# Kernel tuning notes

Hardware: AMD Instinct MI355X
Metric: run time of the kernel (lower is better)

Reference implementation:

```python
import jax, jax.numpy as jnp
import numpy as np

WS = (2, 6, 12)            # window (z, h, w)
DIM = 192
HEADS = 6
Z_WINS = 8 // WS[0]        # 4
H_WINS = 96 // WS[1]       # 16
W_WINS = 180 // WS[2]      # 15
NUM_WINDOWS = Z_WINS * H_WINS  # 64 (bias-sharing groups)


def _position_index(ws):
    # Faithful numpy port of define_3d_earth_position_index (Pangu-Weather).
    z, h, w = ws
    czi = np.arange(z)
    czj = -np.arange(z) * z
    chi = np.arange(h)
    chj = -np.arange(h) * h
    cw = np.arange(w)
    c1 = np.stack(np.meshgrid(czi, chi, cw, indexing='ij')).reshape(3, -1)
    c2 = np.stack(np.meshgrid(czj, chj, cw, indexing='ij')).reshape(3, -1)
    coords = (c1[:, :, None] - c2[:, None, :]).transpose(1, 2, 0).astype(np.int64)
    coords[:, :, 2] += w - 1
    coords[:, :, 1] *= 2 * w - 1
    coords[:, :, 0] *= (2 * w - 1) * h * h
    return coords.sum(-1).astype(np.int32)  # (L, L)


def setup_inputs() -> dict:
    key = jax.random.key(0)
    ks = jax.random.split(key, 6)
    L = WS[0] * WS[1] * WS[2]                 # 144
    total = NUM_WINDOWS * W_WINS              # 960 windows (b=1)
    table_len = (2 * WS[2] - 1) * WS[1] ** 2 * WS[0] ** 2  # 3312
    x = jax.random.normal(ks[0], (total, L, DIM), jnp.float32)
    mask = jax.random.normal(ks[1], (total, L, L), jnp.float32)
    W1 = jax.random.normal(ks[2], (DIM, 3 * DIM), jnp.float32) * 0.02
    b1 = jnp.zeros((3 * DIM,), jnp.float32)
    W2 = jax.random.normal(ks[3], (DIM, DIM), jnp.float32) * 0.02
    b2 = jnp.zeros((DIM,), jnp.float32)
    bias_table = jax.random.normal(ks[4], (table_len, NUM_WINDOWS, HEADS), jnp.float32) * 0.02
    position_index = jnp.asarray(_position_index(WS))
    return {"x": x, "mask": mask, "W1": W1, "b1": b1, "W2": W2, "b2": b2,
            "bias_table": bias_table, "position_index": position_index,
            "b": 1, "z": Z_WINS, "h": H_WINS}


def reference(x, mask, W1, b1, W2, b2, bias_table, position_index, b, z, h):
    B_, L, C = x.shape                     # (b*nw*w_wins, 144, 192)
    hd = C // HEADS
    scale = hd ** -0.5
    nw = bias_table.shape[1]

    qkv = (x @ W1 + b1).reshape(B_, L, 3, HEADS, hd)
    qkv = qkv.transpose(2, 0, 3, 1, 4)      # (3, B_, H, L, hd)
    q, k, v = qkv[0] * scale, qkv[1], qkv[2]

    attn = jnp.einsum('bhld,bhmd->bhlm', q, k)  # (B_, H, L, L)

    # Earth-specific bias: gather then (nw, H, L, L)
    bias = bias_table[position_index]           # (L, L, nw, H)
    bias = bias.transpose(2, 3, 0, 1)           # (nw, H, L, L)

    # window ordering is (b, nw, w_wins); bias broadcasts over w_wins
    attn = attn.reshape(b, nw, -1, HEADS, L, L) + bias[None, :, None]
    attn = attn.reshape(b, -1, HEADS, L, L)
    attn = attn + mask[None, :, None]           # mask: (total, L, L)
    attn = attn.reshape(B_, HEADS, L, L)

    attn = jax.nn.softmax(attn, axis=-1)        # dropout p=0.0 -> identity

    out = jnp.einsum('bhlm,bhmd->bhld', attn, v)
    out = out.transpose(0, 2, 1, 3).reshape(B_, L, C)
    out = out @ W2 + b2
    return out
```

## Files before the change

kernel.cpp:

```cpp
#include <hip/hip_runtime.h>
#include <hip/hip_bf16.h>

typedef __bf16 bf16_t;
typedef __attribute__((ext_vector_type(8))) __bf16 bf16x8;
typedef __attribute__((ext_vector_type(4))) __bf16 bf16x4;
typedef __attribute__((ext_vector_type(4))) float f32x4;

#define LQ 144
#define CDIM 192
#define NHEADS 6
#define HD 32
#define NWIN 960
#define WWINS 15
#define MROWS 138240
#define SCALE_Q 0.17677669529663687f

#define OFF_QKV   0ull
#define OFF_ATTN  159252480ull
#define OFF_BIAS  212336640ull
#define OFF_W1T   244187136ull
#define OFF_W2T   244408320ull

__global__ void prep_w_kernel(const float* __restrict__ W1, const float* __restrict__ W2,
                              bf16_t* __restrict__ w1t, bf16_t* __restrict__ w2t) {
    int idx = blockIdx.x * 256 + threadIdx.x;
    if (idx < 576 * 192) {
        int n = idx / 192, k = idx % 192;
        w1t[idx] = (bf16_t)W1[k * 576 + n];
    }
    if (idx < 192 * 192) {
        int n = idx / 192, k = idx % 192;
        w2t[idx] = (bf16_t)W2[k * 192 + n];
    }
}

__global__ void bias_gather_kernel(const float* __restrict__ table, const int* __restrict__ pi,
                                   float* __restrict__ bias_full) {
    int idx = blockIdx.x * 256 + threadIdx.x;
    int m = idx % LQ;
    int t = idx / LQ;
    int q = t % LQ; t /= LQ;
    int hh = t % NHEADS;
    int nw = t / NHEADS;
    int p = pi[q * LQ + m];
    bias_full[idx] = table[(p * 64 + nw) * NHEADS + hh];
}

__global__ __launch_bounds__(256) void gemm1_kernel(
    const float* __restrict__ X, const bf16_t* __restrict__ W1t,
    const float* __restrict__ b1, bf16_t* __restrict__ qkv) {
    __shared__ bf16_t As[128 * 72];
    __shared__ bf16_t Bs[64 * 72];
    const int tid = threadIdx.x;
    const int row0 = blockIdx.x * 128;
    const int n0 = blockIdx.y * 64;
    const int lane = tid & 63, wid = tid >> 6;
    const int wr = wid >> 1, wc = wid & 1;
    const int l15 = lane & 15, g = lane >> 4;

    f32x4 acc[4][2];
#pragma unroll
    for (int a = 0; a < 4; ++a)
#pragma unroll
        for (int b = 0; b < 2; ++b) acc[a][b] = (f32x4){0.f, 0.f, 0.f, 0.f};

    for (int kk = 0; kk < 3; ++kk) {
        {
            int row = tid >> 1, half = tid & 1;
            const float* src = X + (size_t)(row0 + row) * 192 + kk * 64 + half * 32;
            bf16_t* dst = &As[row * 72 + half * 32];
#pragma unroll
            for (int j = 0; j < 4; ++j) {
                f32x4 v0 = ((const f32x4*)src)[2 * j];
                f32x4 v1 = ((const f32x4*)src)[2 * j + 1];
                bf16x8 w;
#pragma unroll
                for (int r = 0; r < 4; ++r) { w[r] = (bf16_t)v0[r]; w[4 + r] = (bf16_t)v1[r]; }
                *(bf16x8*)(dst + 8 * j) = w;
            }
        }
        {
            int n = tid >> 2, qtr = tid & 3;
            const bf16_t* src = W1t + (size_t)(n0 + n) * 192 + kk * 64 + qtr * 16;
            bf16x8 v0 = ((const bf16x8*)src)[0];
            bf16x8 v1 = ((const bf16x8*)src)[1];
            *(bf16x8*)&Bs[n * 72 + qtr * 16] = v0;
            *(bf16x8*)&Bs[n * 72 + qtr * 16 + 8] = v1;
        }
        __syncthreads();
#pragma unroll
        for (int ks = 0; ks < 2; ++ks) {
            bf16x8 af[4], bfr[2];
#pragma unroll
            for (int rt = 0; rt < 4; ++rt)
                af[rt] = *(const bf16x8*)&As[(wr * 64 + rt * 16 + l15) * 72 + ks * 32 + 8 * g];
#pragma unroll
            for (int ct = 0; ct < 2; ++ct)
                bfr[ct] = *(const bf16x8*)&Bs[(wc * 32 + ct * 16 + l15) * 72 + ks * 32 + 8 * g];
#pragma unroll
            for (int rt = 0; rt < 4; ++rt)
#pragma unroll
                for (int ct = 0; ct < 2; ++ct)
                    acc[rt][ct] = __builtin_amdgcn_mfma_f32_16x16x32_bf16(af[rt], bfr[ct], acc[rt][ct], 0, 0, 0);
        }
        __syncthreads();
    }
#pragma unroll
    for (int ct = 0; ct < 2; ++ct) {
        int n = n0 + wc * 32 + ct * 16 + l15;
        float bv = b1[n];
        float sc = (n < 192) ? SCALE_Q : 1.0f;
#pragma unroll
        for (int rt = 0; rt < 4; ++rt) {
#pragma unroll
            for (int r = 0; r < 4; ++r) {
                int m = row0 + wr * 64 + rt * 16 + 4 * g + r;
                qkv[(size_t)m * 576 + n] = (bf16_t)((acc[rt][ct][r] + bv) * sc);
            }
        }
    }
}

#define QKP 40
#define PP 168
__global__ __launch_bounds__(192) void attn_kernel(
    const bf16_t* __restrict__ qkv, const float* __restrict__ mask,
    const float* __restrict__ bias_full, bf16_t* __restrict__ attn_o) {
    __shared__ bf16_t Vt[32 * PP];
    __shared__ bf16_t Pb[144 * PP];
    bf16_t* Qs = Pb;
    bf16_t* Ks = Pb + 144 * QKP;

    const int tid = threadIdx.x;
    const int bid = blockIdx.x;
    const int wi = bid / NHEADS;
    const int h = bid % NHEADS;
    const int gb = (wi / WWINS) * NHEADS + h;

    const bf16_t* base = qkv + (size_t)wi * (LQ * 576);
#pragma unroll
    for (int it = 0; it < 3; ++it) {
        int idx = tid + it * 192;
        int l = idx >> 2, sg = (idx & 3) * 8;
        const bf16_t* p = base + l * 576 + h * 32 + sg;
        bf16x8 vq = *(const bf16x8*)(p);
        bf16x8 vk = *(const bf16x8*)(p + 192);
        bf16x8 vv = *(const bf16x8*)(p + 384);
        *(bf16x8*)&Qs[l * QKP + sg] = vq;
        *(bf16x8*)&Ks[l * QKP + sg] = vk;
#pragma unroll
        for (int j = 0; j < 8; ++j) Vt[(sg + j) * PP + l] = vv[j];
    }
    for (int idx = tid; idx < 512; idx += 192)
        Vt[(idx >> 4) * PP + 144 + (idx & 15)] = (bf16_t)0.f;
    __syncthreads();

    const int lane = tid & 63;
    const int wid = tid >> 6;
    const int l15 = lane & 15;
    const int g = lane >> 4;
    const int q0w = wid * 48;

    bf16x8 qf[3];
#pragma unroll
    for (int qt = 0; qt < 3; ++qt)
        qf[qt] = *(const bf16x8*)&Qs[(q0w + qt * 16 + l15) * QKP + 8 * g];

    f32x4 acc[3][9];
#pragma unroll
    for (int qt = 0; qt < 3; ++qt)
#pragma unroll
        for (int mt = 0; mt < 9; ++mt) acc[qt][mt] = (f32x4){0.f, 0.f, 0.f, 0.f};

#pragma unroll
    for (int mt = 0; mt < 9; ++mt) {
        bf16x8 kf = *(const bf16x8*)&Ks[(mt * 16 + l15) * QKP + 8 * g];
#pragma unroll
        for (int qt = 0; qt < 3; ++qt)
            acc[qt][mt] = __builtin_amdgcn_mfma_f32_16x16x32_bf16(kf, qf[qt], acc[qt][mt], 0, 0, 0);
    }
#pragma unroll
    for (int qt = 0; qt < 3; ++qt) {
        int q = q0w + qt * 16 + l15;
        const f32x4* brow = (const f32x4*)(bias_full + ((size_t)gb * LQ + q) * LQ);
        const f32x4* mrow = (const f32x4*)(mask + ((size_t)wi * LQ + q) * LQ);
#pragma unroll
        for (int mt = 0; mt < 9; ++mt) {
            f32x4 bv = brow[mt * 4 + g];
            f32x4 mv = mrow[mt * 4 + g];
            acc[qt][mt] += bv + mv;
        }
    }
    __syncthreads();

#pragma unroll
    for (int qt = 0; qt < 3; ++qt) {
        float mx = -3.0e38f;
#pragma unroll
        for (int mt = 0; mt < 9; ++mt)
#pragma unroll
            for (int r = 0; r < 4; ++r) mx = fmaxf(mx, acc[qt][mt][r]);
        mx = fmaxf(mx, __shfl_xor(mx, 16));
        mx = fmaxf(mx, __shfl_xor(mx, 32));
        float sum = 0.f;
#pragma unroll
        for (int mt = 0; mt < 9; ++mt)
#pragma unroll
            for (int r = 0; r < 4; ++r) {
                float e = __expf(acc[qt][mt][r] - mx);
                acc[qt][mt][r] = e;
                sum += e;
            }
        sum += __shfl_xor(sum, 16);
        sum += __shfl_xor(sum, 32);
        float inv = 1.f / sum;
        int q = q0w + qt * 16 + l15;
#pragma unroll
        for (int mt = 0; mt < 9; ++mt) {
            bf16x4 pk;
#pragma unroll
            for (int r = 0; r < 4; ++r) pk[r] = (bf16_t)(acc[qt][mt][r] * inv);
            *(bf16x4*)&Pb[q * PP + mt * 16 + 4 * g] = pk;
        }
    }
    {
        bf16x4 z; 
#pragma unroll
        for (int r = 0; r < 4; ++r) z[r] = (bf16_t)0.f;
#pragma unroll
        for (int u = 0; u < 3; ++u) {
            int uu = lane + u * 64;
            int row = q0w + (uu >> 2);
            *(bf16x4*)&Pb[row * PP + 144 + (uu & 3) * 4] = z;
        }
    }
    __syncthreads();

    f32x4 o[2][3];
#pragma unroll
    for (int dt = 0; dt < 2; ++dt)
#pragma unroll
        for (int qt = 0; qt < 3; ++qt) o[dt][qt] = (f32x4){0.f, 0.f, 0.f, 0.f};
#pragma unroll
    for (int mc = 0; mc < 5; ++mc) {
        bf16x8 av[2], bp[3];
#pragma unroll
        for (int dt = 0; dt < 2; ++dt)
            av[dt] = *(const bf16x8*)&Vt[(dt * 16 + l15) * PP + mc * 32 + 8 * g];
#pragma unroll
        for (int qt = 0; qt < 3; ++qt)
            bp[qt] = *(const bf16x8*)&Pb[(q0w + qt * 16 + l15) * PP + mc * 32 + 8 * g];
#pragma unroll
        for (int dt = 0; dt < 2; ++dt)
#pragma unroll
            for (int qt = 0; qt < 3; ++qt)
                o[dt][qt] = __builtin_amdgcn_mfma_f32_16x16x32_bf16(av[dt], bp[qt], o[dt][qt], 0, 0, 0);
    }
#pragma unroll
    for (int dt = 0; dt < 2; ++dt)
#pragma unroll
        for (int qt = 0; qt < 3; ++qt) {
            int q = q0w + qt * 16 + l15;
            int d0 = dt * 16 + 4 * g;
            bf16x4 pk;
#pragma unroll
            for (int r = 0; r < 4; ++r) pk[r] = (bf16_t)o[dt][qt][r];
            *(bf16x4*)(attn_o + ((size_t)wi * LQ + q) * CDIM + h * HD + d0) = pk;
        }
}

__global__ __launch_bounds__(256) void gemm2_kernel(
    const bf16_t* __restrict__ A, const bf16_t* __restrict__ W2t,
    const float* __restrict__ b2, float* __restrict__ out) {
    __shared__ bf16_t As[128 * 72];
    __shared__ bf16_t Bs[64 * 72];
    const int tid = threadIdx.x;
    const int row0 = blockIdx.x * 128;
    const int n0 = blockIdx.y * 64;
    const int lane = tid & 63, wid = tid >> 6;
    const int wr = wid >> 1, wc = wid & 1;
    const int l15 = lane & 15, g = lane >> 4;

    f32x4 acc[4][2];
#pragma unroll
    for (int a = 0; a < 4; ++a)
#pragma unroll
        for (int b = 0; b < 2; ++b) acc[a][b] = (f32x4){0.f, 0.f, 0.f, 0.f};

    for (int kk = 0; kk < 3; ++kk) {
        {
            int row = tid >> 1, half = tid & 1;
            const bf16_t* src = A + (size_t)(row0 + row) * 192 + kk * 64 + half * 32;
            bf16_t* dst = &As[row * 72 + half * 32];
            bf16x8 v0 = ((const bf16x8*)src)[0];
            bf16x8 v1 = ((const bf16x8*)src)[1];
            bf16x8 v2 = ((const bf16x8*)src)[2];
            bf16x8 v3 = ((const bf16x8*)src)[3];
            *(bf16x8*)(dst) = v0; *(bf16x8*)(dst + 8) = v1;
            *(bf16x8*)(dst + 16) = v2; *(bf16x8*)(dst + 24) = v3;
        }
        {
            int n = tid >> 2, qtr = tid & 3;
            const bf16_t* src = W2t + (size_t)(n0 + n) * 192 + kk * 64 + qtr * 16;
            bf16x8 v0 = ((const bf16x8*)src)[0];
            bf16x8 v1 = ((const bf16x8*)src)[1];
            *(bf16x8*)&Bs[n * 72 + qtr * 16] = v0;
            *(bf16x8*)&Bs[n * 72 + qtr * 16 + 8] = v1;
        }
        __syncthreads();
#pragma unroll
        for (int ks = 0; ks < 2; ++ks) {
            bf16x8 af[4], bfr[2];
#pragma unroll
            for (int rt = 0; rt < 4; ++rt)
                af[rt] = *(const bf16x8*)&As[(wr * 64 + rt * 16 + l15) * 72 + ks * 32 + 8 * g];
#pragma unroll
            for (int ct = 0; ct < 2; ++ct)
                bfr[ct] = *(const bf16x8*)&Bs[(wc * 32 + ct * 16 + l15) * 72 + ks * 32 + 8 * g];
#pragma unroll
            for (int rt = 0; rt < 4; ++rt)
#pragma unroll
                for (int ct = 0; ct < 2; ++ct)
                    acc[rt][ct] = __builtin_amdgcn_mfma_f32_16x16x32_bf16(af[rt], bfr[ct], acc[rt][ct], 0, 0, 0);
        }
        __syncthreads();
    }
#pragma unroll
    for (int ct = 0; ct < 2; ++ct) {
        int n = n0 + wc * 32 + ct * 16 + l15;
        float bv = b2[n];
#pragma unroll
        for (int rt = 0; rt < 4; ++rt) {
#pragma unroll
            for (int r = 0; r < 4; ++r) {
                int m = row0 + wr * 64 + rt * 16 + 4 * g + r;
                out[(size_t)m * 192 + n] = acc[rt][ct][r] + bv;
            }
        }
    }
}

extern "C" void kernel_launch(void* const* d_in, const int* in_sizes, int n_in,
                              void* d_out, int out_size, void* d_ws, size_t ws_size,
                              hipStream_t stream) {
    const float* x = (const float*)d_in[0];
    const float* mask = (const float*)d_in[1];
    const float* W1 = (const float*)d_in[2];
    const float* b1 = (const float*)d_in[3];
    const float* W2 = (const float*)d_in[4];
    const float* b2 = (const float*)d_in[5];
    const float* table = (const float*)d_in[6];
    const int* pi = (const int*)d_in[7];
    float* out = (float*)d_out;

    char* ws = (char*)d_ws;
    bf16_t* qkv = (bf16_t*)(ws + OFF_QKV);
    bf16_t* attn_o = (bf16_t*)(ws + OFF_ATTN);
    float* bias_full = (float*)(ws + OFF_BIAS);
    bf16_t* w1t = (bf16_t*)(ws + OFF_W1T);
    bf16_t* w2t = (bf16_t*)(ws + OFF_W2T);

    prep_w_kernel<<<dim3(432), dim3(256), 0, stream>>>(W1, W2, w1t, w2t);
    bias_gather_kernel<<<dim3(31104), dim3(256), 0, stream>>>(table, pi, bias_full);
    gemm1_kernel<<<dim3(1080, 9), dim3(256), 0, stream>>>(x, w1t, b1, qkv);
    attn_kernel<<<dim3(5760), dim3(192), 0, stream>>>(qkv, mask, bias_full, attn_o);
    gemm2_kernel<<<dim3(1080, 3), dim3(256), 0, stream>>>(attn_o, w2t, b2, out);
}
```

Baseline: 699.5 us.

## Split attention block into nine waves, one 16-row query tile each

The attention kernel now launches 576 threads (9 waves) per window-head, so each wave handles one 16-row query tile instead of three. Q fragments are loaded straight from global memory into registers rather than staged through shared memory, and K and V are loaded by all threads in a single pass. The aim is to raise the number of waves available to hide the latency of the bias and mask global loads and the softmax, and to lower per-thread register use. The cost is more barrier participants per block and fewer MFMAs per wave to amortize shared-memory fragment loads.

```diff
diff --git a/kernel.cpp b/kernel.cpp
--- a/kernel.cpp
+++ b/kernel.cpp
@@ -121,85 +121,66 @@
     }
 }
 
-#define QKP 40
+#define KP 40
 #define PP 168
-__global__ __launch_bounds__(192) void attn_kernel(
+__global__ __launch_bounds__(576) void attn_kernel(
     const bf16_t* __restrict__ qkv, const float* __restrict__ mask,
     const float* __restrict__ bias_full, bf16_t* __restrict__ attn_o) {
-    __shared__ bf16_t Vt[32 * PP];
-    __shared__ bf16_t Pb[144 * PP];
-    bf16_t* Qs = Pb;
-    bf16_t* Ks = Pb + 144 * QKP;
+    __shared__ bf16_t smem[176 * PP];
+    bf16_t* Pb = smem;
+    bf16_t* Vt = smem + 144 * PP;
+    bf16_t* Ks = smem;
 
     const int tid = threadIdx.x;
     const int bid = blockIdx.x;
     const int wi = bid / NHEADS;
     const int h = bid % NHEADS;
     const int gb = (wi / WWINS) * NHEADS + h;
-
     const bf16_t* base = qkv + (size_t)wi * (LQ * 576);
-#pragma unroll
-    for (int it = 0; it < 3; ++it) {
-        int idx = tid + it * 192;
-        int l = idx >> 2, sg = (idx & 3) * 8;
-        const bf16_t* p = base + l * 576 + h * 32 + sg;
-        bf16x8 vq = *(const bf16x8*)(p);
-        bf16x8 vk = *(const bf16x8*)(p + 192);
-        bf16x8 vv = *(const bf16x8*)(p + 384);
-        *(bf16x8*)&Qs[l * QKP + sg] = vq;
-        *(bf16x8*)&Ks[l * QKP + sg] = vk;
+
+    {
+        int l = tid >> 2, sg = (tid & 3) * 8;
+        const bf16_t* p = base + l * 576 + 192 + h * HD + sg;
+        bf16x8 vk = *(const bf16x8*)(p);
+        bf16x8 vv = *(const bf16x8*)(p + 192);
+        *(bf16x8*)&Ks[l * KP + sg] = vk;
 #pragma unroll
         for (int j = 0; j < 8; ++j) Vt[(sg + j) * PP + l] = vv[j];
     }
-    for (int idx = tid; idx < 512; idx += 192)
-        Vt[(idx >> 4) * PP + 144 + (idx & 15)] = (bf16_t)0.f;
-    __syncthreads();
+    if (tid < 512) Vt[(tid >> 4) * PP + 144 + (tid & 15)] = (bf16_t)0.f;
 
     const int lane = tid & 63;
     const int wid = tid >> 6;
     const int l15 = lane & 15;
     const int g = lane >> 4;
-    const int q0w = wid * 48;
-
-    bf16x8 qf[3];
-#pragma unroll
-    for (int qt = 0; qt < 3; ++qt)
-        qf[qt] = *(const bf16x8*)&Qs[(q0w + qt * 16 + l15) * QKP + 8 * g];
-
-    f32x4 acc[3][9];
-#pragma unroll
-    for (int qt = 0; qt < 3; ++qt)
-#pragma unroll
-        for (int mt = 0; mt < 9; ++mt) acc[qt][mt] = (f32x4){0.f, 0.f, 0.f, 0.f};
-
+    const int q = wid * 16 + l15;
+
+    bf16x8 qf = *(const bf16x8*)(base + q * 576 + h * HD + 8 * g);
+    __syncthreads();
+
+    f32x4 acc[9];
+#pragma unroll
+    for (int mt = 0; mt < 9; ++mt) acc[mt] = (f32x4){0.f, 0.f, 0.f, 0.f};
 #pragma unroll
     for (int mt = 0; mt < 9; ++mt) {
-        bf16x8 kf = *(const bf16x8*)&Ks[(mt * 16 + l15) * QKP + 8 * g];
-#pragma unroll
-        for (int qt = 0; qt < 3; ++qt)
-            acc[qt][mt] = __builtin_amdgcn_mfma_f32_16x16x32_bf16(kf, qf[qt], acc[qt][mt], 0, 0, 0);
-    }
-#pragma unroll
-    for (int qt = 0; qt < 3; ++qt) {
-        int q = q0w + qt * 16 + l15;
+        bf16x8 kf = *(const bf16x8*)&Ks[(mt * 16 + l15) * KP + 8 * g];
+        acc[mt] = __builtin_amdgcn_mfma_f32_16x16x32_bf16(kf, qf, acc[mt], 0, 0, 0);
+    }
+    {
         const f32x4* brow = (const f32x4*)(bias_full + ((size_t)gb * LQ + q) * LQ);
         const f32x4* mrow = (const f32x4*)(mask + ((size_t)wi * LQ + q) * LQ);
 #pragma unroll
-        for (int mt = 0; mt < 9; ++mt) {
-            f32x4 bv = brow[mt * 4 + g];
-            f32x4 mv = mrow[mt * 4 + g];
-            acc[qt][mt] += bv + mv;
-        }
+        for (int mt = 0; mt < 9; ++mt)
+            acc[mt] += brow[mt * 4 + g] + mrow[mt * 4 + g];
     }
     __syncthreads();
 
-#pragma unroll
-    for (int qt = 0; qt < 3; ++qt) {
+    {
         float mx = -3.0e38f;
 #pragma unroll
         for (int mt = 0; mt < 9; ++mt)
 #pragma unroll
-            for (int r = 0; r < 4; ++r) mx = fmaxf(mx, acc[qt][mt][r]);
+            for (int r = 0; r < 4; ++r) mx = fmaxf(mx, acc[mt][r]);
         mx = fmaxf(mx, __shfl_xor(mx, 16));
         mx = fmaxf(mx, __shfl_xor(mx, 32));
         float sum = 0.f;
@@ -207,66 +188,49 @@
         for (int mt = 0; mt < 9; ++mt)
 #pragma unroll
             for (int r = 0; r < 4; ++r) {
-                float e = __expf(acc[qt][mt][r] - mx);
-                acc[qt][mt][r] = e;
+                float e = __expf(acc[mt][r] - mx);
+                acc[mt][r] = e;
                 sum += e;
             }
         sum += __shfl_xor(sum, 16);
         sum += __shfl_xor(sum, 32);
         float inv = 1.f / sum;
-        int q = q0w + qt * 16 + l15;
 #pragma unroll
         for (int mt = 0; mt < 9; ++mt) {
             bf16x4 pk;
 #pragma unroll
-            for (int r = 0; r < 4; ++r) pk[r] = (bf16_t)(acc[qt][mt][r] * inv);
+            for (int r = 0; r < 4; ++r) pk[r] = (bf16_t)(acc[mt][r] * inv);
             *(bf16x4*)&Pb[q * PP + mt * 16 + 4 * g] = pk;
         }
     }
     {
-        bf16x4 z; 
+        bf16x4 z;
 #pragma unroll
         for (int r = 0; r < 4; ++r) z[r] = (bf16_t)0.f;
-#pragma unroll
-        for (int u = 0; u < 3; ++u) {
-            int uu = lane + u * 64;
-            int row = q0w + (uu >> 2);
-            *(bf16x4*)&Pb[row * PP + 144 + (uu & 3) * 4] = z;
-        }
+        int row = wid * 16 + (lane >> 2);
+        *(bf16x4*)&Pb[row * PP + 144 + (lane & 3) * 4] = z;
     }
     __syncthreads();
 
-    f32x4 o[2][3];
-#pragma unroll
-    for (int dt = 0; dt < 2; ++dt)
-#pragma unroll
-        for (int qt = 0; qt < 3; ++qt) o[dt][qt] = (f32x4){0.f, 0.f, 0.f, 0.f};
+    f32x4 o[2];
+#pragma unroll
+    for (int dt = 0; dt < 2; ++dt) o[dt] = (f32x4){0.f, 0.f, 0.f, 0.f};
 #pragma unroll
     for (int mc = 0; mc < 5; ++mc) {
-        bf16x8 av[2], bp[3];
-#pragma unroll
-        for (int dt = 0; dt < 2; ++dt)
-            av[dt] = *(const bf16x8*)&Vt[(dt * 16 + l15) * PP + mc * 32 + 8 * g];
-#pragma unroll
-        for (int qt = 0; qt < 3; ++qt)
-            bp[qt] = *(const bf16x8*)&Pb[(q0w + qt * 16 + l15) * PP + mc * 32 + 8 * g];
-#pragma unroll
-        for (int dt = 0; dt < 2; ++dt)
-#pragma unroll
-            for (int qt = 0; qt < 3; ++qt)
-                o[dt][qt] = __builtin_amdgcn_mfma_f32_16x16x32_bf16(av[dt], bp[qt], o[dt][qt], 0, 0, 0);
-    }
-#pragma unroll
-    for (int dt = 0; dt < 2; ++dt)
-#pragma unroll
-        for (int qt = 0; qt < 3; ++qt) {
-            int q = q0w + qt * 16 + l15;
-            int d0 = dt * 16 + 4 * g;
-            bf16x4 pk;
-#pragma unroll
-            for (int r = 0; r < 4; ++r) pk[r] = (bf16_t)o[dt][qt][r];
-            *(bf16x4*)(attn_o + ((size_t)wi * LQ + q) * CDIM + h * HD + d0) = pk;
-        }
+        bf16x8 bp = *(const bf16x8*)&Pb[q * PP + mc * 32 + 8 * g];
+#pragma unroll
+        for (int dt = 0; dt < 2; ++dt) {
+            bf16x8 av = *(const bf16x8*)&Vt[(dt * 16 + l15) * PP + mc * 32 + 8 * g];
+            o[dt] = __builtin_amdgcn_mfma_f32_16x16x32_bf16(av, bp, o[dt], 0, 0, 0);
+        }
+    }
+#pragma unroll
+    for (int dt = 0; dt < 2; ++dt) {
+        bf16x4 pk;
+#pragma unroll
+        for (int r = 0; r < 4; ++r) pk[r] = (bf16_t)o[dt][r];
+        *(bf16x4*)(attn_o + ((size_t)wi * LQ + q) * CDIM + h * HD + dt * 16 + 4 * g) = pk;
+    }
 }
 
 __global__ __launch_bounds__(256) void gemm2_kernel(
@@ -363,6 +327,6 @@
     prep_w_kernel<<<dim3(432), dim3(256), 0, stream>>>(W1, W2, w1t, w2t);
     bias_gather_kernel<<<dim3(31104), dim3(256), 0, stream>>>(table, pi, bias_full);
     gemm1_kernel<<<dim3(1080, 9), dim3(256), 0, stream>>>(x, w1t, b1, qkv);
-    attn_kernel<<<dim3(5760), dim3(192), 0, stream>>>(qkv, mask, bias_full, attn_o);
+    attn_kernel<<<dim3(5760), dim3(576), 0, stream>>>(qkv, mask, bias_full, attn_o);
     gemm2_kernel<<<dim3(1080, 3), dim3(256), 0, stream>>>(attn_o, w2t, b2, out);
 }
```

After: 654.5 us. -6.4%, faster.
